# Optimization experiments

Measured on AMD Instinct MI355X. Metric: run time of the kernel, lower is better.

Reference implementation:

```python
import jax, jax.numpy as jnp
import numpy as np


def setup_inputs() -> dict:
    key = jax.random.key(0)
    kx, ka, kw, kk = jax.random.split(key, 4)
    N, F, D, K = 4096, 256, 128, 2
    X = jax.random.normal(kx, (N, F), dtype=jnp.float32)
    # K+1 dense adjacency/distance matrices; uniform(0,1) keeps degrees positive
    adj = jax.random.uniform(ka, (K + 1, N, N), dtype=jnp.float32)
    W_emb = jax.random.normal(kw, (F, D), dtype=jnp.float32) / np.float32(np.sqrt(F))
    kernels = jax.random.normal(kk, (K + 1, F, D), dtype=jnp.float32) / np.float32(np.sqrt(F))
    alpha = jnp.float32(0.1)
    return {"X": X, "adj": adj, "W_emb": W_emb, "kernels": kernels, "alpha": alpha}


def reference(X, adj, W_emb, kernels, alpha):
    # X: [N,F], adj: [K+1,N,N], W_emb: [F,D], kernels: [K+1,F,D], alpha: scalar
    E = X @ W_emb                                # [N,D] learned embeddings
    low_rank = alpha * (E @ E.T)                 # [N,N] rank-D correction, shared across hops
    XK = jnp.einsum('nf,kfd->knd', X, kernels)   # [K+1,N,D] hop-wise kernel projections
    out = jnp.zeros((X.shape[0], kernels.shape[-1]), dtype=X.dtype)
    for hop in range(adj.shape[0]):              # small fixed K+1 loop
        A_hat = adj[hop] + low_rank              # [N,N]
        d = jax.lax.rsqrt(jnp.sum(A_hat, axis=1))  # deg^{-1/2}; diag-matmul == broadcast scale
        A_norm = d[:, None] * A_hat * d[None, :]  # D^{-1/2} A_hat D^{-1/2}
        out = out + A_norm @ XK[hop]
    return jax.nn.relu(out)
```

## Files before the change

### kernel.cpp

```cpp
#include <hip/hip_runtime.h>
#include <hip/hip_bf16.h>

#define Nn 4096
#define Fdim 256
#define Ddim 128
#define NH 3

typedef __bf16 bf16x8 __attribute__((ext_vector_type(8)));
typedef float f32x4 __attribute__((ext_vector_type(4)));
typedef unsigned short ushort8v __attribute__((ext_vector_type(8)));
typedef unsigned short ushort4v __attribute__((ext_vector_type(4)));

#define MFMA(a, b, c) __builtin_amdgcn_mfma_f32_16x16x32_bf16((a), (b), (c), 0, 0, 0)

__device__ __forceinline__ float bf2f(unsigned short u) {
    union { unsigned int i; float f; } cv;
    cv.i = ((unsigned int)u) << 16;
    return cv.f;
}
__device__ __forceinline__ unsigned short f2bf(float f) {
    union { __bf16 b; unsigned short u; } cv;
    cv.b = (__bf16)f;
    return cv.u;
}
__device__ __forceinline__ bf16x8 cvt8(const float* p, float s) {
    const float4 lo = *(const float4*)p;
    const float4 hi = *(const float4*)(p + 4);
    bf16x8 r;
    r[0] = (__bf16)(lo.x * s); r[1] = (__bf16)(lo.y * s);
    r[2] = (__bf16)(lo.z * s); r[3] = (__bf16)(lo.w * s);
    r[4] = (__bf16)(hi.x * s); r[5] = (__bf16)(hi.y * s);
    r[6] = (__bf16)(hi.z * s); r[7] = (__bf16)(hi.w * s);
    return r;
}

__global__ void kprobe(const unsigned short* __restrict__ X, float* __restrict__ mode,
                       float* __restrict__ s) {
    int t = threadIdx.x;
    s[t] = 0.f;
    s[t + 64] = 0.f;
    int wild = 0;
    for (int i = t; i < 2048; i += 64) {
        unsigned short u = X[i];
        int e = (u >> 7) & 0xFF;
        if (e >= 132) wild = 1;
    }
    unsigned long long m = __ballot(wild != 0);
    if (t == 0) mode[0] = (__popcll(m) > 4) ? 0.0f : 1.0f;
}

__global__ void k0_wt(const void* __restrict__ W_emb, const void* __restrict__ kernels,
                      unsigned short* __restrict__ WT, const float* __restrict__ mode) {
    bool isbf = mode[0] > 0.5f;
    int b = blockIdx.x, nt = b >> 1, fh = b & 1;
    __shared__ unsigned short T[128][136];
    int t = threadIdx.x;
    int d4 = t & 31, fr = t >> 5;
    if (isbf) {
        const unsigned short* Wsrc = (nt == 0) ? (const unsigned short*)W_emb
                                               : ((const unsigned short*)kernels + (size_t)(nt - 1) * Fdim * Ddim);
        for (int p = 0; p < 16; ++p) {
            int fl = fr + 8 * p;
            int f = fh * 128 + fl;
            ushort4v v = *(const ushort4v*)(Wsrc + (size_t)f * Ddim + 4 * d4);
            T[4 * d4 + 0][fl] = v[0]; T[4 * d4 + 1][fl] = v[1];
            T[4 * d4 + 2][fl] = v[2]; T[4 * d4 + 3][fl] = v[3];
        }
    } else {
        const float* Wsrc = (nt == 0) ? (const float*)W_emb
                                      : ((const float*)kernels + (size_t)(nt - 1) * Fdim * Ddim);
        for (int p = 0; p < 16; ++p) {
            int fl = fr + 8 * p;
            int f = fh * 128 + fl;
            float4 v = *(const float4*)(Wsrc + (size_t)f * Ddim + 4 * d4);
            T[4 * d4 + 0][fl] = f2bf(v.x); T[4 * d4 + 1][fl] = f2bf(v.y);
            T[4 * d4 + 2][fl] = f2bf(v.z); T[4 * d4 + 3][fl] = f2bf(v.w);
        }
    }
    __syncthreads();
    int f4 = t & 31, dr = t >> 5;
    for (int p = 0; p < 16; ++p) {
        int dd = dr + 8 * p;
        ushort4v w;
        w[0] = T[dd][4 * f4 + 0]; w[1] = T[dd][4 * f4 + 1];
        w[2] = T[dd][4 * f4 + 2]; w[3] = T[dd][4 * f4 + 3];
        *(ushort4v*)(WT + (size_t)nt * Ddim * Fdim + (size_t)dd * Fdim + fh * 128 + 4 * f4) = w;
    }
}

__global__ void k1_proj(const void* __restrict__ Xv, const unsigned short* __restrict__ WT,
                        float* __restrict__ E, float* __restrict__ XK, float* __restrict__ s,
                        const float* __restrict__ mode) {
    bool isbf = mode[0] > 0.5f;
    int mt = blockIdx.x >> 2, nt = blockIdx.x & 3;
    int t = threadIdx.x, wid = t >> 6, lane = t & 63, l15 = lane & 15, q = lane >> 4;
    int m0 = mt * 16;
    const unsigned short* BT = WT + (size_t)nt * Ddim * Fdim;
    const unsigned short* b0p = BT + (size_t)(wid * 32 + l15) * Fdim;
    const unsigned short* b1p = b0p + 16 * Fdim;
    f32x4 acc0 = {0.f, 0.f, 0.f, 0.f}, acc1 = {0.f, 0.f, 0.f, 0.f};
    if (isbf) {
        const unsigned short* Arow = (const unsigned short*)Xv + (size_t)(m0 + l15) * Fdim;
#pragma unroll
        for (int ks = 0; ks < 8; ++ks) {
            int kk = ks * 32 + q * 8;
            bf16x8 a = *(const bf16x8*)(Arow + kk);
            bf16x8 b0 = *(const bf16x8*)(b0p + kk);
            bf16x8 b1 = *(const bf16x8*)(b1p + kk);
            acc0 = MFMA(a, b0, acc0);
            acc1 = MFMA(a, b1, acc1);
        }
    } else {
        const float* Arow = (const float*)Xv + (size_t)(m0 + l15) * Fdim;
#pragma unroll
        for (int ks = 0; ks < 8; ++ks) {
            int kk = ks * 32 + q * 8;
            bf16x8 a = cvt8(Arow + kk, 1.0f);
            bf16x8 b0 = *(const bf16x8*)(b0p + kk);
            bf16x8 b1 = *(const bf16x8*)(b1p + kk);
            acc0 = MFMA(a, b0, acc0);
            acc1 = MFMA(a, b1, acc1);
        }
    }
    float* dst = (nt == 0) ? E : (XK + (size_t)(nt - 1) * Nn * Ddim);
#pragma unroll
    for (int r = 0; r < 4; ++r) {
        int ml = q * 4 + r;
        dst[(size_t)(m0 + ml) * Ddim + wid * 32 + l15] = acc0[r];
        dst[(size_t)(m0 + ml) * Ddim + wid * 32 + 16 + l15] = acc1[r];
    }
    if (nt == 0) {
        float c0 = acc0[0] + acc0[1] + acc0[2] + acc0[3];
        float c1 = acc1[0] + acc1[1] + acc1[2] + acc1[3];
        c0 += __shfl_xor(c0, 16, 64); c0 += __shfl_xor(c0, 32, 64);
        c1 += __shfl_xor(c1, 16, 64); c1 += __shfl_xor(c1, 32, 64);
        if (q == 0) {
            atomicAdd(&s[wid * 32 + l15], c0);
            atomicAdd(&s[wid * 32 + 16 + l15], c1);
        }
    }
}

__global__ void k2_rowsum(const void* __restrict__ adjv, float* __restrict__ rowsum,
                          const float* __restrict__ mode) {
    bool isbf = mode[0] > 0.5f;
    int t = threadIdx.x, w = t >> 6, lane = t & 63;
    int r = blockIdx.x * 4 + w;
    float sum = 0.f;
    if (isbf) {
        const unsigned short* rp = (const unsigned short*)adjv + (size_t)r * Nn;
#pragma unroll
        for (int it = 0; it < 8; ++it) {
            ushort8v v = *(const ushort8v*)(rp + (it * 64 + lane) * 8);
            sum += bf2f(v[0]) + bf2f(v[1]) + bf2f(v[2]) + bf2f(v[3]) +
                   bf2f(v[4]) + bf2f(v[5]) + bf2f(v[6]) + bf2f(v[7]);
        }
    } else {
        const float4* rp = (const float4*)((const float*)adjv + (size_t)r * Nn);
#pragma unroll
        for (int it = 0; it < 16; ++it) {
            float4 v = rp[it * 64 + lane];
            sum += v.x + v.y + v.z + v.w;
        }
    }
#pragma unroll
    for (int off = 32; off > 0; off >>= 1) sum += __shfl_down(sum, off, 64);
    if (lane == 0) rowsum[r] = sum;
}

__global__ void k4_dgen(const float* __restrict__ E, const float* __restrict__ rowsum,
                        const float* __restrict__ s, const void* __restrict__ alphap,
                        float* __restrict__ dbuf, const float* __restrict__ mode) {
    bool isbf = mode[0] > 0.5f;
    __shared__ float ss[128];
    int t = threadIdx.x;
    if (t < 128) ss[t] = s[t];
    __syncthreads();
    int wid = t >> 6, lane = t & 63;
    int node = blockIdx.x * 32 + wid * 8 + (lane >> 3);
    int sub = lane & 7;
    const float4* er = (const float4*)(E + (size_t)node * Ddim + sub * 16);
    float acc = 0.f;
#pragma unroll
    for (int k = 0; k < 4; ++k) {
        float4 v = er[k];
        int c = sub * 16 + 4 * k;
        acc += v.x * ss[c] + v.y * ss[c + 1] + v.z * ss[c + 2] + v.w * ss[c + 3];
    }
#pragma unroll
    for (int off = 1; off < 8; off <<= 1) acc += __shfl_xor(acc, off, 64);
    if (sub == 0) {
        float a = isbf ? bf2f(((const unsigned short*)alphap)[0]) : ((const float*)alphap)[0];
#pragma unroll
        for (int h = 0; h < NH; ++h)
            dbuf[h * Nn + node] = rsqrtf(rowsum[h * Nn + node] + a * acc);
    }
}

__global__ void k5_transpose(const float* __restrict__ XK, const float* __restrict__ E,
                             const float* __restrict__ dbuf, unsigned short* __restrict__ Yp,
                             unsigned short* __restrict__ ET) {
    __shared__ unsigned short T[128][72];
    __shared__ float sl[64];
    int b = blockIdx.x, t = threadIdx.x;
    bool isET = (b >= 192);
    int h = 0, jt;
    const float* src;
    if (!isET) { h = b >> 6; jt = b & 63; src = XK + (size_t)h * Nn * Ddim; }
    else { jt = b - 192; src = E; }
    if (t < 64) sl[t] = isET ? 1.0f : dbuf[h * Nn + jt * 64 + t];
    __syncthreads();
    int d4 = t & 31, jr = t >> 5;
    for (int p = 0; p < 8; ++p) {
        int j = jr + 8 * p;
        float4 v = *(const float4*)(src + (size_t)(jt * 64 + j) * Ddim + 4 * d4);
        float sc = sl[j];
        T[4 * d4 + 0][j] = f2bf(v.x * sc); T[4 * d4 + 1][j] = f2bf(v.y * sc);
        T[4 * d4 + 2][j] = f2bf(v.z * sc); T[4 * d4 + 3][j] = f2bf(v.w * sc);
    }
    __syncthreads();
    int jj4 = t & 15, nr = t >> 4;
    unsigned short* dst = isET ? ET : (Yp + (size_t)h * Ddim * Nn);
    for (int p = 0; p < 8; ++p) {
        int n = nr + 16 * p;
        ushort4v w;
        w[0] = T[n][4 * jj4 + 0]; w[1] = T[n][4 * jj4 + 1];
        w[2] = T[n][4 * jj4 + 2]; w[3] = T[n][4 * jj4 + 3];
        int j = jt * 64 + 4 * jj4;
        *(ushort4v*)(dst + (size_t)n * Nn + j) = w;
    }
}

__global__ void k6_mgen(const unsigned short* __restrict__ ET,
                        const unsigned short* __restrict__ Yp, float* __restrict__ Mpart) {
    int b = blockIdx.x;
    int kc = b / 24, rem = b % 24, h = rem >> 3, mtm = rem & 7;
    int t = threadIdx.x, wid = t >> 6, lane = t & 63, l15 = lane & 15, q = lane >> 4;
    int m0 = mtm * 16;
    const unsigned short* Ar = ET + (size_t)(m0 + l15) * Nn + kc * 512;
    const unsigned short* Yph = Yp + (size_t)h * Ddim * Nn;
    const unsigned short* bb = Yph + (size_t)(wid * 32 + l15) * Nn + kc * 512 + q * 8;
    f32x4 acc0 = {0.f, 0.f, 0.f, 0.f}, acc1 = {0.f, 0.f, 0.f, 0.f};
#pragma unroll 4
    for (int ks = 0; ks < 16; ++ks) {
        bf16x8 a = *(const bf16x8*)(Ar + ks * 32 + q * 8);
        bf16x8 b0 = *(const bf16x8*)(bb + ks * 32);
        bf16x8 b1 = *(const bf16x8*)(bb + (size_t)16 * Nn + ks * 32);
        acc0 = MFMA(a, b0, acc0);
        acc1 = MFMA(a, b1, acc1);
    }
    float* out = Mpart + (size_t)kc * (NH * Ddim * Ddim) + (size_t)h * (Ddim * Ddim);
#pragma unroll
    for (int r = 0; r < 4; ++r) {
        int ml = q * 4 + r;
        out[(m0 + ml) * Ddim + wid * 32 + l15] = acc0[r];
        out[(m0 + ml) * Ddim + wid * 32 + 16 + l15] = acc1[r];
    }
}

__global__ void k6b_mred(const float* __restrict__ Mpart, unsigned short* __restrict__ MT) {
    int idx = blockIdx.x * 256 + threadIdx.x;
    int d2 = idx / 384, kcol = idx % 384;
    int h = kcol >> 7, d1 = kcol & 127;
    float sum = 0.f;
#pragma unroll
    for (int kc = 0; kc < 8; ++kc)
        sum += Mpart[(size_t)kc * (NH * Ddim * Ddim) + h * (Ddim * Ddim) + d1 * Ddim + d2];
    MT[idx] = f2bf(sum);
}

__global__ void k8_lgen(const float* __restrict__ E, const float* __restrict__ dbuf,
                        const void* __restrict__ alphap, const unsigned short* __restrict__ MT,
                        float* __restrict__ L, const float* __restrict__ mode) {
    bool isbf = mode[0] > 0.5f;
    int mt = blockIdx.x;
    int t = threadIdx.x, wid = t >> 6, lane = t & 63, l15 = lane & 15, q = lane >> 4;
    int m0 = mt * 16, m = m0 + l15;
    float a = isbf ? bf2f(((const unsigned short*)alphap)[0]) : ((const float*)alphap)[0];
    float dv[NH];
#pragma unroll
    for (int h = 0; h < NH; ++h) dv[h] = a * dbuf[h * Nn + m];
    const float* Er = E + (size_t)m * Ddim;
    const unsigned short* b0p = MT + (size_t)(wid * 32 + l15) * 384;
    const unsigned short* b1p = b0p + 16 * 384;
    f32x4 acc0 = {0.f, 0.f, 0.f, 0.f}, acc1 = {0.f, 0.f, 0.f, 0.f};
#pragma unroll
    for (int ks = 0; ks < 12; ++ks) {
        int kk = ks * 32;
        int h = kk >> 7;
        int kloc = (kk & 127) + q * 8;
        bf16x8 aa = cvt8(Er + kloc, dv[h]);
        bf16x8 b0 = *(const bf16x8*)(b0p + kk + q * 8);
        bf16x8 b1 = *(const bf16x8*)(b1p + kk + q * 8);
        acc0 = MFMA(aa, b0, acc0);
        acc1 = MFMA(aa, b1, acc1);
    }
#pragma unroll
    for (int r = 0; r < 4; ++r) {
        int ml = q * 4 + r;
        L[(size_t)(m0 + ml) * Ddim + wid * 32 + l15] = acc0[r];
        L[(size_t)(m0 + ml) * Ddim + wid * 32 + 16 + l15] = acc1[r];
    }
}

__global__ void __launch_bounds__(512, 1) k7_fused(const void* __restrict__ adjv,
        const unsigned short* __restrict__ Yp, const float* __restrict__ dbuf,
        float* __restrict__ Pp, const float* __restrict__ mode) {
    bool isbf = mode[0] > 0.5f;
    __shared__ unsigned short lds[2][6][4096];
    __shared__ float dsh[NH][128];
    int b = blockIdx.x;
    int mt = b >> 3, kc = b & 7;
    int m0 = mt * 128;
    int kbase = kc * 512;
    int t = threadIdx.x;
    if (t < 384) { int h = t >> 7, m = t & 127; dsh[h][m] = dbuf[h * Nn + m0 + m]; }

    int sr = t >> 2, ss = t & 3;
    int sw = ss ^ ((sr >> 2) & 3);
    const float* aBaseF = (const float*)adjv + (size_t)(m0 + sr) * Nn + kbase + 8 * sw;
    const unsigned short* aBaseH = (const unsigned short*)adjv + (size_t)(m0 + sr) * Nn + kbase + 8 * sw;
    const unsigned short* bBase = Yp + (size_t)sr * Nn + kbase + 8 * sw;

    int wid = t >> 6, lane = t & 63, l15 = lane & 15, q = lane >> 4;
    int wm = wid >> 1, wn = wid & 1;
    f32x4 acc[NH][2][4] = {};

    float4 ApF[NH][2];
    ushort8v ApH[NH];
    ushort8v Bpr[NH];

    auto stage_load = [&](int c) {
        int ko = c * 32;
        if (isbf) {
#pragma unroll
            for (int h = 0; h < NH; ++h)
                ApH[h] = *(const ushort8v*)(aBaseH + (size_t)h * Nn * Nn + ko);
        } else {
#pragma unroll
            for (int h = 0; h < NH; ++h) {
                ApF[h][0] = *(const float4*)(aBaseF + (size_t)h * Nn * Nn + ko);
                ApF[h][1] = *(const float4*)(aBaseF + (size_t)h * Nn * Nn + ko + 4);
            }
        }
#pragma unroll
        for (int h = 0; h < NH; ++h)
            Bpr[h] = *(const ushort8v*)(bBase + (size_t)h * Ddim * Nn + ko);
    };
    auto stage_write = [&](int buf) {
#pragma unroll
        for (int h = 0; h < NH; ++h) {
            ushort8v w;
            if (isbf) w = ApH[h];
            else {
                w[0] = f2bf(ApF[h][0].x); w[1] = f2bf(ApF[h][0].y);
                w[2] = f2bf(ApF[h][0].z); w[3] = f2bf(ApF[h][0].w);
                w[4] = f2bf(ApF[h][1].x); w[5] = f2bf(ApF[h][1].y);
                w[6] = f2bf(ApF[h][1].z); w[7] = f2bf(ApF[h][1].w);
            }
            *(ushort8v*)&lds[buf][h][t * 8] = w;
            *(ushort8v*)&lds[buf][3 + h][t * 8] = Bpr[h];
        }
    };
    auto compute = [&](int buf) {
#pragma unroll
        for (int h = 0; h < NH; ++h) {
            bf16x8 af[2], bfr[4];
#pragma unroll
            for (int i = 0; i < 2; ++i) {
                int m = wm * 32 + i * 16 + l15;
                af[i] = *(const bf16x8*)&lds[buf][h][m * 32 + (q ^ ((m >> 2) & 3)) * 8];
            }
#pragma unroll
            for (int j = 0; j < 4; ++j) {
                int n = wn * 64 + j * 16 + l15;
                bfr[j] = *(const bf16x8*)&lds[buf][3 + h][n * 32 + (q ^ ((n >> 2) & 3)) * 8];
            }
#pragma unroll
            for (int i = 0; i < 2; ++i)
#pragma unroll
                for (int j = 0; j < 4; ++j)
                    acc[h][i][j] = MFMA(af[i], bfr[j], acc[h][i][j]);
        }
    };

    stage_load(0);
    stage_write(0);
    __syncthreads();
#pragma unroll 2
    for (int c = 0; c < 16; ++c) {
        if (c < 15) stage_load(c + 1);
        compute(c & 1);
        if (c < 15) {
            stage_write((c + 1) & 1);
            __syncthreads();
        }
    }

    float* Pk = Pp + (size_t)kc * (Nn * Ddim);
#pragma unroll
    for (int i = 0; i < 2; ++i) {
#pragma unroll
        for (int r = 0; r < 4; ++r) {
            int row = wm * 32 + i * 16 + q * 4 + r;
            float d0 = dsh[0][row], d1 = dsh[1][row], d2 = dsh[2][row];
            float* pr = Pk + (size_t)(m0 + row) * Ddim + wn * 64 + l15;
#pragma unroll
            for (int j = 0; j < 4; ++j) {
                float v = d0 * acc[0][i][j][r] + d1 * acc[1][i][j][r] + d2 * acc[2][i][j][r];
                pr[j * 16] = v;
            }
        }
    }
}

__global__ void k9_combine(const float* __restrict__ Pp, const float* __restrict__ L,
                           void* __restrict__ outv, const float* __restrict__ mode) {
    bool isbf = mode[0] > 0.5f;
    size_t base = ((size_t)blockIdx.x * 256 + threadIdx.x) * 4;
    float4 a = *(const float4*)(L + base);
    float r0 = a.x, r1 = a.y, r2 = a.z, r3 = a.w;
#pragma unroll
    for (int kc = 0; kc < 8; ++kc) {
        float4 v = *(const float4*)(Pp + (size_t)kc * (Nn * Ddim) + base);
        r0 += v.x; r1 += v.y; r2 += v.z; r3 += v.w;
    }
    r0 = r0 > 0.f ? r0 : 0.f;
    r1 = r1 > 0.f ? r1 : 0.f;
    r2 = r2 > 0.f ? r2 : 0.f;
    r3 = r3 > 0.f ? r3 : 0.f;
    if (isbf) {
        ushort4v w;
        w[0] = f2bf(r0); w[1] = f2bf(r1); w[2] = f2bf(r2); w[3] = f2bf(r3);
        *(ushort4v*)((unsigned short*)outv + base) = w;
    } else {
        float4 w; w.x = r0; w.y = r1; w.z = r2; w.w = r3;
        *(float4*)((float*)outv + base) = w;
    }
}

extern "C" void kernel_launch(void* const* d_in, const int* in_sizes, int n_in,
                              void* d_out, int out_size, void* d_ws, size_t ws_size,
                              hipStream_t stream) {
    const void* X = d_in[0];
    const void* adj = d_in[1];
    const void* W_emb = d_in[2];
    const void* kernels = d_in[3];
    const void* alphap = d_in[4];

    float* E = (float*)d_ws;
    float* XK = E + 524288;
    float* rowsum = XK + 1572864;
    float* s = rowsum + 12288;
    float* dbuf = s + 128;
    float* Mpart = dbuf + 12288;
    float* L = Mpart + 393216;
    float* Pp = L + 524288;
    unsigned short* WT = (unsigned short*)(Pp + 8 * 524288);
    unsigned short* ET = WT + 131072;
    unsigned short* Yp = ET + 524288;
    unsigned short* MT = Yp + 1572864;
    float* modef = (float*)(MT + 49152);

    kprobe<<<1, 64, 0, stream>>>((const unsigned short*)X, modef, s);
    k0_wt<<<8, 256, 0, stream>>>(W_emb, kernels, WT, modef);
    k1_proj<<<1024, 256, 0, stream>>>(X, WT, E, XK, s, modef);
    k2_rowsum<<<3072, 256, 0, stream>>>(adj, rowsum, modef);
    k4_dgen<<<128, 256, 0, stream>>>(E, rowsum, s, alphap, dbuf, modef);
    k5_transpose<<<256, 256, 0, stream>>>(XK, E, dbuf, Yp, ET);
    k6_mgen<<<192, 256, 0, stream>>>(ET, Yp, Mpart);
    k6b_mred<<<192, 256, 0, stream>>>(Mpart, MT);
    k8_lgen<<<256, 256, 0, stream>>>(E, dbuf, alphap, MT, L, modef);
    k7_fused<<<256, 512, 0, stream>>>(adj, Yp, dbuf, Pp, modef);
    k9_combine<<<512, 256, 0, stream>>>(Pp, L, d_out, modef);
}
```

Before: 388.1 us.

## Fuse split-K combine into main GEMM via last-block counter, double-buffer register prefetch

Removes the separate combine kernel by having the last of the 8 split-K blocks for each row tile, found through an atomic counter, sum the partials plus L, apply ReLU and write the output. The main loop also now holds two register stages of global prefetch, with loads issued two chunks ahead, to hide more load latency. This saves a kernel launch and one pass over the partial buffer. In exchange it adds fences and atomics, and the extra prefetch registers could spill under the 512-thread launch bound.

```diff
diff --git a/kernel.cpp b/kernel.cpp
--- a/kernel.cpp
+++ b/kernel.cpp
@@ -35,10 +35,11 @@
 }
 
 __global__ void kprobe(const unsigned short* __restrict__ X, float* __restrict__ mode,
-                       float* __restrict__ s) {
+                       float* __restrict__ s, int* __restrict__ ctr) {
     int t = threadIdx.x;
     s[t] = 0.f;
     s[t + 64] = 0.f;
+    if (t < 32) ctr[t] = 0;
     int wild = 0;
     for (int i = t; i < 2048; i += 64) {
         unsigned short u = X[i];
@@ -305,10 +306,12 @@
 
 __global__ void __launch_bounds__(512, 1) k7_fused(const void* __restrict__ adjv,
         const unsigned short* __restrict__ Yp, const float* __restrict__ dbuf,
-        float* __restrict__ Pp, const float* __restrict__ mode) {
+        float* __restrict__ Pp, const float* __restrict__ L, void* __restrict__ outv,
+        int* __restrict__ ctr, const float* __restrict__ mode) {
     bool isbf = mode[0] > 0.5f;
     __shared__ unsigned short lds[2][6][4096];
     __shared__ float dsh[NH][128];
+    __shared__ int lastFlag;
     int b = blockIdx.x;
     int mt = b >> 3, kc = b & 7;
     int m0 = mt * 128;
@@ -326,40 +329,39 @@
     int wm = wid >> 1, wn = wid & 1;
     f32x4 acc[NH][2][4] = {};
 
-    float4 ApF[NH][2];
-    ushort8v ApH[NH];
-    ushort8v Bpr[NH];
-
-    auto stage_load = [&](int c) {
+    float4 AF0[NH][2], AF1[NH][2];
+    ushort8v AH0[NH], AH1[NH], BR0[NH], BR1[NH];
+
+    auto stage_load = [&](float4 (&AF)[NH][2], ushort8v (&AH)[NH], ushort8v (&BR)[NH], int c) {
         int ko = c * 32;
         if (isbf) {
 #pragma unroll
             for (int h = 0; h < NH; ++h)
-                ApH[h] = *(const ushort8v*)(aBaseH + (size_t)h * Nn * Nn + ko);
+                AH[h] = *(const ushort8v*)(aBaseH + (size_t)h * Nn * Nn + ko);
         } else {
 #pragma unroll
             for (int h = 0; h < NH; ++h) {
-                ApF[h][0] = *(const float4*)(aBaseF + (size_t)h * Nn * Nn + ko);
-                ApF[h][1] = *(const float4*)(aBaseF + (size_t)h * Nn * Nn + ko + 4);
+                AF[h][0] = *(const float4*)(aBaseF + (size_t)h * Nn * Nn + ko);
+                AF[h][1] = *(const float4*)(aBaseF + (size_t)h * Nn * Nn + ko + 4);
             }
         }
 #pragma unroll
         for (int h = 0; h < NH; ++h)
-            Bpr[h] = *(const ushort8v*)(bBase + (size_t)h * Ddim * Nn + ko);
+            BR[h] = *(const ushort8v*)(bBase + (size_t)h * Ddim * Nn + ko);
     };
-    auto stage_write = [&](int buf) {
+    auto stage_write = [&](float4 (&AF)[NH][2], ushort8v (&AH)[NH], ushort8v (&BR)[NH], int buf) {
 #pragma unroll
         for (int h = 0; h < NH; ++h) {
             ushort8v w;
-            if (isbf) w = ApH[h];
+            if (isbf) w = AH[h];
             else {
-                w[0] = f2bf(ApF[h][0].x); w[1] = f2bf(ApF[h][0].y);
-                w[2] = f2bf(ApF[h][0].z); w[3] = f2bf(ApF[h][0].w);
-                w[4] = f2bf(ApF[h][1].x); w[5] = f2bf(ApF[h][1].y);
-                w[6] = f2bf(ApF[h][1].z); w[7] = f2bf(ApF[h][1].w);
+                w[0] = f2bf(AF[h][0].x); w[1] = f2bf(AF[h][0].y);
+                w[2] = f2bf(AF[h][0].z); w[3] = f2bf(AF[h][0].w);
+                w[4] = f2bf(AF[h][1].x); w[5] = f2bf(AF[h][1].y);
+                w[6] = f2bf(AF[h][1].z); w[7] = f2bf(AF[h][1].w);
             }
             *(ushort8v*)&lds[buf][h][t * 8] = w;
-            *(ushort8v*)&lds[buf][3 + h][t * 8] = Bpr[h];
+            *(ushort8v*)&lds[buf][3 + h][t * 8] = BR[h];
         }
     };
     auto compute = [&](int buf) {
@@ -384,15 +386,21 @@
         }
     };
 
-    stage_load(0);
-    stage_write(0);
-    __syncthreads();
-#pragma unroll 2
-    for (int c = 0; c < 16; ++c) {
-        if (c < 15) stage_load(c + 1);
-        compute(c & 1);
-        if (c < 15) {
-            stage_write((c + 1) & 1);
+    stage_load(AF0, AH0, BR0, 0);
+    stage_load(AF1, AH1, BR1, 1);
+    stage_write(AF0, AH0, BR0, 0);
+    __syncthreads();
+
+    for (int cc = 0; cc < 8; ++cc) {
+        int c0 = 2 * cc;
+        if (cc < 7) stage_load(AF0, AH0, BR0, c0 + 2);
+        compute(0);
+        stage_write(AF1, AH1, BR1, 1);
+        __syncthreads();
+        if (cc < 7) stage_load(AF1, AH1, BR1, c0 + 3);
+        compute(1);
+        if (cc < 7) {
+            stage_write(AF0, AH0, BR0, 0);
             __syncthreads();
         }
     }
@@ -412,30 +420,40 @@
             }
         }
     }
-}
-
-__global__ void k9_combine(const float* __restrict__ Pp, const float* __restrict__ L,
-                           void* __restrict__ outv, const float* __restrict__ mode) {
-    bool isbf = mode[0] > 0.5f;
-    size_t base = ((size_t)blockIdx.x * 256 + threadIdx.x) * 4;
-    float4 a = *(const float4*)(L + base);
-    float r0 = a.x, r1 = a.y, r2 = a.z, r3 = a.w;
-#pragma unroll
-    for (int kc = 0; kc < 8; ++kc) {
-        float4 v = *(const float4*)(Pp + (size_t)kc * (Nn * Ddim) + base);
-        r0 += v.x; r1 += v.y; r2 += v.z; r3 += v.w;
-    }
-    r0 = r0 > 0.f ? r0 : 0.f;
-    r1 = r1 > 0.f ? r1 : 0.f;
-    r2 = r2 > 0.f ? r2 : 0.f;
-    r3 = r3 > 0.f ? r3 : 0.f;
-    if (isbf) {
-        ushort4v w;
-        w[0] = f2bf(r0); w[1] = f2bf(r1); w[2] = f2bf(r2); w[3] = f2bf(r3);
-        *(ushort4v*)((unsigned short*)outv + base) = w;
-    } else {
-        float4 w; w.x = r0; w.y = r1; w.z = r2; w.w = r3;
-        *(float4*)((float*)outv + base) = w;
+
+    __threadfence();
+    if (t == 0) {
+        int prev = atomicAdd(&ctr[mt], 1);
+        lastFlag = (prev == 7) ? 1 : 0;
+    }
+    __syncthreads();
+    if (lastFlag) {
+        __threadfence();
+        int row = m0 + (t >> 2);
+        int c0 = (t & 3) * 32;
+#pragma unroll
+        for (int g = 0; g < 8; ++g) {
+            size_t off = (size_t)row * Ddim + c0 + g * 4;
+            float4 a = *(const float4*)(L + off);
+            float r0 = a.x, r1 = a.y, r2 = a.z, r3 = a.w;
+#pragma unroll
+            for (int k2 = 0; k2 < 8; ++k2) {
+                float4 v = *(const float4*)(Pp + (size_t)k2 * (Nn * Ddim) + off);
+                r0 += v.x; r1 += v.y; r2 += v.z; r3 += v.w;
+            }
+            r0 = r0 > 0.f ? r0 : 0.f;
+            r1 = r1 > 0.f ? r1 : 0.f;
+            r2 = r2 > 0.f ? r2 : 0.f;
+            r3 = r3 > 0.f ? r3 : 0.f;
+            if (isbf) {
+                ushort4v w;
+                w[0] = f2bf(r0); w[1] = f2bf(r1); w[2] = f2bf(r2); w[3] = f2bf(r3);
+                *(ushort4v*)((unsigned short*)outv + off) = w;
+            } else {
+                float4 w; w.x = r0; w.y = r1; w.z = r2; w.w = r3;
+                *(float4*)((float*)outv + off) = w;
+            }
+        }
     }
 }
 
@@ -461,8 +479,9 @@
     unsigned short* Yp = ET + 524288;
     unsigned short* MT = Yp + 1572864;
     float* modef = (float*)(MT + 49152);
-
-    kprobe<<<1, 64, 0, stream>>>((const unsigned short*)X, modef, s);
+    int* ctr = (int*)(modef + 1);
+
+    kprobe<<<1, 64, 0, stream>>>((const unsigned short*)X, modef, s, ctr);
     k0_wt<<<8, 256, 0, stream>>>(W_emb, kernels, WT, modef);
     k1_proj<<<1024, 256, 0, stream>>>(X, WT, E, XK, s, modef);
     k2_rowsum<<<3072, 256, 0, stream>>>(adj, rowsum, modef);
@@ -471,6 +490,5 @@
     k6_mgen<<<192, 256, 0, stream>>>(ET, Yp, Mpart);
     k6b_mred<<<192, 256, 0, stream>>>(Mpart, MT);
     k8_lgen<<<256, 256, 0, stream>>>(E, dbuf, alphap, MT, L, modef);
-    k7_fused<<<256, 512, 0, stream>>>(adj, Yp, dbuf, Pp, modef);
-    k9_combine<<<512, 256, 0, stream>>>(Pp, L, d_out, modef);
-}
+    k7_fused<<<256, 512, 0, stream>>>(adj, Yp, dbuf, Pp, L, d_out, ctr, modef);
+}
```

After: 505.0 us. +30.1%, slower.
